# Optimization experiments

Hardware: AMD Instinct MI355X
Metric: run time of the kernel (lower is better)

Reference implementation:

```python
import jax, jax.numpy as jnp
import numpy as np

N = 50000      # nodes
E = 600000     # edges
DIN = 128      # dim_in
DOUT = 128     # dim_out (mulhead=1)
DG = 64        # dim_gate


def setup_inputs() -> dict:
    key = jax.random.key(0)
    ks = jax.random.split(key, 10)
    rows = jax.random.randint(ks[0], (E,), 0, N, dtype=jnp.int32)   # dest nodes
    cols = jax.random.randint(ks[1], (E,), 0, N, dtype=jnp.int32)   # src nodes
    vals = jax.random.uniform(ks[2], (E,), dtype=jnp.float32)       # adj_norm values
    feat = jax.random.normal(ks[3], (N, DIN), dtype=jnp.float32)
    s = 1.0 / np.sqrt(DIN)
    W0 = jax.random.normal(ks[4], (DIN, DOUT), dtype=jnp.float32) * s
    b0 = jnp.zeros((DOUT,), dtype=jnp.float32)
    W1 = jax.random.normal(ks[5], (DIN, DOUT), dtype=jnp.float32) * s
    b1 = jnp.zeros((DOUT,), dtype=jnp.float32)
    att = jax.random.normal(ks[6], (2 * DOUT,), dtype=jnp.float32) * 0.1  # attention param [1, 2*DOUT] flattened
    W_pool = jax.random.normal(ks[7], (DIN, DG), dtype=jnp.float32) * s    # weight_pool_gate
    W_gate = jax.random.normal(ks[8], (2 * DIN + DG, 1), dtype=jnp.float32) * 0.05  # weight_gate, mulhead=1
    offset0 = jnp.zeros((DOUT,), dtype=jnp.float32)
    scale0 = jnp.ones((DOUT,), dtype=jnp.float32)
    offset1 = jnp.zeros((DOUT,), dtype=jnp.float32)
    scale1 = jnp.ones((DOUT,), dtype=jnp.float32)
    return dict(rows=rows, cols=cols, vals=vals, feat=feat, W0=W0, b0=b0,
                W1=W1, b1=b1, att=att, W_pool=W_pool, W_gate=W_gate,
                offset0=offset0, scale0=scale0, offset1=offset1, scale1=scale1)


def _batch_norm(x, scale, offset):
    # per-node norm over the feature dim (unbiased=False), matching _batch_norm
    m = x.mean(axis=1, keepdims=True)
    v = x.var(axis=1, keepdims=True) + 1e-9
    return (x - m) * scale * jax.lax.rsqrt(v) + offset


def reference(rows, cols, vals, feat, W0, b0, W1, b1, att, W_pool, W_gate,
              offset0, scale0, offset1, scale1):
    n = feat.shape[0]
    d = W0.shape[1]
    # --- gate value (GaAN eq. 3) ---
    zj = feat @ W_pool                                   # [N, DG]
    neigh_zj = jax.ops.segment_max(zj[cols], rows, num_segments=n)  # per-row max over neighbors
    neigh_zj = jnp.where(jnp.isfinite(neigh_zj), neigh_zj, 0.0)     # empty rows -> zeros
    neigh_mean = jax.ops.segment_sum(vals[:, None] * feat[cols], rows, num_segments=n)  # spmm(adj, feat)
    gate = jnp.concatenate([feat, neigh_zj, neigh_mean], axis=1) @ W_gate  # [N, 1]
    # --- per-order feature transforms (order=1, mulhead=1) ---
    h0 = jax.nn.relu(feat @ W0 + b0)                     # order 0 (self)
    h1 = jax.nn.relu(feat @ W1 + b1)                     # order 1 (neighbor)
    # --- sparse attention aggregation ---
    a_self = jax.nn.leaky_relu(h0 @ att[:d], 0.2)        # [N]
    a_neigh = jax.nn.leaky_relu(h1 @ att[d:], 0.2)       # [N]
    e = a_self[rows] + a_neigh[cols]                     # per-edge score (replaces adj values)
    agg = jax.ops.segment_sum(e[:, None] * h1[cols], rows, num_segments=n)  # spmm(att_adj, h1)
    agg = agg * gate[:, :1]                              # gated
    # --- per-node batch norm, then 'mean' aggregation (sum of orders) ---
    return _batch_norm(h0, scale0, offset0) + _batch_norm(agg, scale1, offset1)
```

## Files before the change

### kernel.cpp

```cpp
#include <hip/hip_runtime.h>

#define DIN 128
#define DG 64

typedef __attribute__((ext_vector_type(8))) short short8;
typedef __attribute__((ext_vector_type(4))) float f32x4;

static __device__ __forceinline__ unsigned short f2bf(float x) {
    unsigned u = __builtin_bit_cast(unsigned, x);
    u = (u + 0x7FFF + ((u >> 16) & 1)) >> 16;
    return (unsigned short)u;
}
static __device__ __forceinline__ float bf2f(unsigned short s) {
    return __builtin_bit_cast(float, (unsigned)s << 16);
}

__global__ void k_deg(const int* __restrict__ rows, int* __restrict__ deg,
                      int* __restrict__ slot, int E) {
    int e = blockIdx.x * blockDim.x + threadIdx.x;
    if (e < E) slot[e] = atomicAdd(&deg[rows[e]], 1);
}

__global__ __launch_bounds__(1024) void k_scan1(const int* __restrict__ deg,
                                                int* __restrict__ rowptr,
                                                int* __restrict__ bsum, int n) {
    __shared__ int wsum[16];
    __shared__ int woff[16];
    int tid = threadIdx.x;
    int lane = tid & 63, w = tid >> 6;
    int i = blockIdx.x * 1024 + tid;
    int v = (i < n) ? deg[i] : 0;
    int x = v;
    #pragma unroll
    for (int off = 1; off < 64; off <<= 1) {
        int y = __shfl_up(x, off, 64);
        if (lane >= off) x += y;
    }
    if (lane == 63) wsum[w] = x;
    __syncthreads();
    if (w == 0) {
        int t = (lane < 16) ? wsum[lane] : 0;
        int xx = t;
        #pragma unroll
        for (int off = 1; off < 16; off <<= 1) {
            int y = __shfl_up(xx, off, 64);
            if (lane >= off) xx += y;
        }
        if (lane < 16) woff[lane] = xx - t;
    }
    __syncthreads();
    if (i < n) rowptr[i] = x - v + woff[w];
    if (tid == 1023) bsum[blockIdx.x] = woff[15] + wsum[15];
}

__global__ void k_scan2(const int* __restrict__ bsum, int* __restrict__ boff,
                        int* __restrict__ rowptr, int nb, int n) {
    int lane = threadIdx.x;
    int v = (lane < nb) ? bsum[lane] : 0;
    int x = v;
    #pragma unroll
    for (int off = 1; off < 64; off <<= 1) {
        int y = __shfl_up(x, off, 64);
        if (lane >= off) x += y;
    }
    boff[lane] = x - v;
    if (lane == 63) rowptr[n] = x;
}

__global__ void k_scan3(int* __restrict__ rowptr, const int* __restrict__ boff, int n) {
    int i = blockIdx.x * blockDim.x + threadIdx.x;
    if (i < n) rowptr[i] += boff[i >> 10];
}

__global__ __launch_bounds__(256) void k_prep(
    const float* __restrict__ feat, const float* __restrict__ Wg,
    unsigned short* __restrict__ featb,
    float* __restrict__ gpart, float* __restrict__ fdotg, int N, int Npad) {
    int r = blockIdx.x * 4 + (threadIdx.x >> 6);
    int lane = threadIdx.x & 63;
    if (r >= Npad) return;
    if (r >= N) {
        ((ushort2*)(featb + (size_t)r * 128))[lane] = make_ushort2(0, 0);
        return;
    }
    float2 f = ((const float2*)(feat + (size_t)r * 128))[lane];
    ((ushort2*)(featb + (size_t)r * 128))[lane] = make_ushort2(f2bf(f.x), f2bf(f.y));
    float2 G  = ((const float2*)Wg)[lane];
    float2 G2 = ((const float2*)(Wg + 192))[lane];
    float s2 = f.x * G.x + f.y * G.y;
    float s3 = f.x * G2.x + f.y * G2.y;
    #pragma unroll
    for (int off = 32; off; off >>= 1) {
        s2 += __shfl_xor(s2, off, 64);
        s3 += __shfl_xor(s3, off, 64);
    }
    if (lane == 0) { gpart[r] = s2; fdotg[r] = s3; }
}

__global__ __launch_bounds__(256) void k_wt(
    const float* __restrict__ W0, const float* __restrict__ W1,
    unsigned short* __restrict__ Bt) {
    int c = threadIdx.x;
    const float* W = (c < 128) ? W0 : W1;
    int cc = c & 127;
    for (int k = 0; k < 128; ++k)
        Bt[c * 128 + k] = f2bf(W[k * 128 + cc]);
}

#define ALD 136
__global__ __launch_bounds__(256) void k_gemm_mfma(
    const unsigned short* __restrict__ featb, const unsigned short* __restrict__ Bt,
    const float* __restrict__ b0, const float* __restrict__ b1,
    const float* __restrict__ att,
    float* __restrict__ h0, unsigned short* __restrict__ hb,
    float* __restrict__ a_self, float* __restrict__ a_neigh, int N) {
    __shared__ unsigned short As[64 * ALD];
    __shared__ float sredA[128], nredA[128];
    int tid = threadIdx.x;
    int m0 = blockIdx.x * 64;
    for (int i = tid; i < 1024; i += 256) {
        int row = i >> 4, ch = i & 15;
        uint4 v = *(const uint4*)&featb[(size_t)(m0 + row) * 128 + ch * 8];
        *(uint4*)&As[row * ALD + ch * 8] = v;
    }
    __syncthreads();
    int w = tid >> 6, lane = tid & 63;
    int lm = lane & 15, q = lane >> 4;
    f32x4 acc[4][4];
    #pragma unroll
    for (int rt = 0; rt < 4; ++rt)
        #pragma unroll
        for (int ct = 0; ct < 4; ++ct)
            #pragma unroll
            for (int r = 0; r < 4; ++r) acc[rt][ct][r] = 0.f;
    #pragma unroll
    for (int ks = 0; ks < 4; ++ks) {
        short8 a[4], b[4];
        #pragma unroll
        for (int rt = 0; rt < 4; ++rt)
            a[rt] = *(const short8*)&As[(rt * 16 + lm) * ALD + ks * 32 + q * 8];
        #pragma unroll
        for (int ct = 0; ct < 4; ++ct)
            b[ct] = *(const short8*)&Bt[(size_t)(w * 64 + ct * 16 + lm) * 128 + ks * 32 + q * 8];
        #pragma unroll
        for (int rt = 0; rt < 4; ++rt)
            #pragma unroll
            for (int ct = 0; ct < 4; ++ct)
                acc[rt][ct] = __builtin_amdgcn_mfma_f32_16x16x32_bf16(a[rt], b[ct], acc[rt][ct], 0, 0, 0);
    }
    float sacc[4][4];
    #pragma unroll
    for (int rt = 0; rt < 4; ++rt)
        #pragma unroll
        for (int r = 0; r < 4; ++r) sacc[rt][r] = 0.f;
    #pragma unroll
    for (int ct = 0; ct < 4; ++ct) {
        int col = w * 64 + ct * 16 + lm;
        float attc = att[col];
        float bias = (w < 2) ? b0[col] : b1[col - 128];
        #pragma unroll
        for (int rt = 0; rt < 4; ++rt) {
            #pragma unroll
            for (int r = 0; r < 4; ++r) {
                float v = acc[rt][ct][r] + bias;
                v = fmaxf(v, 0.f);
                sacc[rt][r] += v * attc;
                int node = m0 + rt * 16 + q * 4 + r;
                if (node < N) {
                    if (w < 2) h0[(size_t)node * 128 + col] = v;
                    else       hb[(size_t)node * 128 + (col - 128)] = f2bf(v);
                }
            }
        }
    }
    float* red = (w < 2) ? sredA : nredA;
    #pragma unroll
    for (int rt = 0; rt < 4; ++rt)
        #pragma unroll
        for (int r = 0; r < 4; ++r) {
            float s = sacc[rt][r];
            s += __shfl_xor(s, 1, 64); s += __shfl_xor(s, 2, 64);
            s += __shfl_xor(s, 4, 64); s += __shfl_xor(s, 8, 64);
            if (lm == 0) red[(w & 1) * 64 + rt * 16 + q * 4 + r] = s;
        }
    __syncthreads();
    if (tid < 64) {
        int node = m0 + tid;
        if (node < N) {
            float s  = sredA[tid] + sredA[64 + tid];
            float nn = nredA[tid] + nredA[64 + tid];
            a_self[node]  = (s  >= 0.f) ? s  : 0.2f * s;
            a_neigh[node] = (nn >= 0.f) ? nn : 0.2f * nn;
        }
    }
}

#define AS_LD 132
__global__ __launch_bounds__(256) void k_gemm_zj(
    const float* __restrict__ feat, const float* __restrict__ Wp,
    float* __restrict__ zj, int N) {
    __shared__ float As[32 * AS_LD];
    __shared__ float Bs[32 * 64];
    int tid = threadIdx.x;
    int tx = tid & 15, ty = tid >> 4;
    int m0 = blockIdx.x * 128;
    float acc[8][4];
    #pragma unroll
    for (int r = 0; r < 8; ++r)
        #pragma unroll
        for (int c = 0; c < 4; ++c) acc[r][c] = 0.f;
    for (int kc = 0; kc < 128; kc += 32) {
        for (int i = tid; i < 1024; i += 256) {
            int m = i >> 3, kq = (i & 7) << 2;
            int node = m0 + m;
            float4 f;
            if (node < N) f = *(const float4*)&feat[(size_t)node * 128 + kc + kq];
            else          f = make_float4(0.f, 0.f, 0.f, 0.f);
            As[(kq + 0) * AS_LD + m] = f.x;
            As[(kq + 1) * AS_LD + m] = f.y;
            As[(kq + 2) * AS_LD + m] = f.z;
            As[(kq + 3) * AS_LD + m] = f.w;
        }
        for (int i = tid; i < 512; i += 256) {
            int k = i >> 4, cq = (i & 15) << 2;
            *(float4*)&Bs[k * 64 + cq] = *(const float4*)&Wp[(size_t)(kc + k) * 64 + cq];
        }
        __syncthreads();
        #pragma unroll 8
        for (int kk = 0; kk < 32; ++kk) {
            const float* ar = &As[kk * AS_LD];
            float4 a0 = *(const float4*)(ar + 4 * tx);
            float4 a1 = *(const float4*)(ar + 64 + 4 * tx);
            float4 b0v = *(const float4*)&Bs[kk * 64 + 4 * ty];
            float a[8] = {a0.x, a0.y, a0.z, a0.w, a1.x, a1.y, a1.z, a1.w};
            #pragma unroll
            for (int r = 0; r < 8; ++r) {
                acc[r][0] += a[r] * b0v.x; acc[r][1] += a[r] * b0v.y;
                acc[r][2] += a[r] * b0v.z; acc[r][3] += a[r] * b0v.w;
            }
        }
        __syncthreads();
    }
    #pragma unroll
    for (int r = 0; r < 8; ++r) {
        int node = m0 + ((r < 4) ? (4 * tx + r) : (64 + 4 * tx + (r - 4)));
        if (node >= N) continue;
        *(float4*)&zj[(size_t)node * 64 + 4 * ty] =
            make_float4(acc[r][0], acc[r][1], acc[r][2], acc[r][3]);
    }
}

__global__ void k_scatter_meta(const int* __restrict__ rows, const int* __restrict__ cols,
                               const float* __restrict__ vals,
                               const int* __restrict__ rowptr, const int* __restrict__ slot,
                               const float* __restrict__ a_neigh, const float* __restrict__ fdotg,
                               float4* __restrict__ meta, int E) {
    int e = blockIdx.x * blockDim.x + threadIdx.x;
    if (e < E) {
        int c = cols[e];
        int dst = rowptr[rows[e]] + slot[e];
        meta[dst] = make_float4(__builtin_bit_cast(float, c),
                                a_neigh[c], vals[e] * fdotg[c], 0.f);
    }
}

template<int C>
static __device__ __forceinline__ void agg_chunk(
    const float4* __restrict__ meta, int j, int lane, float asr,
    const unsigned short* __restrict__ hb, const float* __restrict__ zj,
    float2& acca, float& zmax, float& vfsum) {
    float4 m[C];
    #pragma unroll
    for (int t = 0; t < C; ++t) m[t] = meta[j + t];
    ushort2 hv[C]; float zv[C];
    #pragma unroll
    for (int t = 0; t < C; ++t) {
        int c = __builtin_bit_cast(int, m[t].x);
        hv[t] = ((const ushort2*)(hb + (size_t)c * 128))[lane];
        zv[t] = zj[(size_t)c * 64 + lane];
    }
    #pragma unroll
    for (int t = 0; t < C; ++t) {
        float es = asr + m[t].y;
        acca.x += es * bf2f(hv[t].x);
        acca.y += es * bf2f(hv[t].y);
        zmax = fmaxf(zmax, zv[t]);
        vfsum += m[t].z;
    }
}

__global__ __launch_bounds__(256) void k_aggregate(
    const float4* __restrict__ meta, const int* __restrict__ rowptr,
    const float* __restrict__ h0, const unsigned short* __restrict__ hb,
    const float* __restrict__ zj,
    const float* __restrict__ a_self, const float* __restrict__ gpart,
    const float* __restrict__ Wg,
    const float* __restrict__ scale0, const float* __restrict__ offset0,
    const float* __restrict__ scale1, const float* __restrict__ offset1,
    float* __restrict__ out, int N) {
    int r = blockIdx.x * 4 + (threadIdx.x >> 6);
    int lane = threadIdx.x & 63;
    if (r >= N) return;
    int jb = rowptr[r], je = rowptr[r + 1];
    float2 acca = {0.f, 0.f};
    float zmax = -__builtin_inff();
    float vfsum = 0.f;
    float asr = a_self[r];
    int j = jb;
    while (j + 8 <= je) { agg_chunk<8>(meta, j, lane, asr, hb, zj, acca, zmax, vfsum); j += 8; }
    if (j + 4 <= je)    { agg_chunk<4>(meta, j, lane, asr, hb, zj, acca, zmax, vfsum); j += 4; }
    while (j < je)      { agg_chunk<1>(meta, j, lane, asr, hb, zj, acca, zmax, vfsum); j += 1; }
    if (jb == je) zmax = 0.f;
    float gs = zmax * Wg[128 + lane];
    #pragma unroll
    for (int off = 32; off; off >>= 1) gs += __shfl_xor(gs, off, 64);
    float gate = gpart[r] + gs + vfsum;
    float2 ag = {acca.x * gate, acca.y * gate};
    float2 x0 = ((const float2*)(h0 + (size_t)r * 128))[lane];
    float m0s = x0.x + x0.y;
    #pragma unroll
    for (int off = 32; off; off >>= 1) m0s += __shfl_xor(m0s, off, 64);
    float m0 = m0s * (1.f / 128.f);
    float d0x = x0.x - m0, d0y = x0.y - m0;
    float v0s = d0x * d0x + d0y * d0y;
    #pragma unroll
    for (int off = 32; off; off >>= 1) v0s += __shfl_xor(v0s, off, 64);
    float inv0 = rsqrtf(v0s * (1.f / 128.f) + 1e-9f);
    float m1s = ag.x + ag.y;
    #pragma unroll
    for (int off = 32; off; off >>= 1) m1s += __shfl_xor(m1s, off, 64);
    float m1 = m1s * (1.f / 128.f);
    float d1x = ag.x - m1, d1y = ag.y - m1;
    float v1s = d1x * d1x + d1y * d1y;
    #pragma unroll
    for (int off = 32; off; off >>= 1) v1s += __shfl_xor(v1s, off, 64);
    float inv1 = rsqrtf(v1s * (1.f / 128.f) + 1e-9f);
    float2 sc0 = ((const float2*)scale0)[lane], of0 = ((const float2*)offset0)[lane];
    float2 sc1 = ((const float2*)scale1)[lane], of1 = ((const float2*)offset1)[lane];
    float2 o;
    o.x = d0x * sc0.x * inv0 + of0.x + d1x * sc1.x * inv1 + of1.x;
    o.y = d0y * sc0.y * inv0 + of0.y + d1y * sc1.y * inv1 + of1.y;
    ((float2*)(out + (size_t)r * 128))[lane] = o;
}

extern "C" void kernel_launch(void* const* d_in, const int* in_sizes, int n_in,
                              void* d_out, int out_size, void* d_ws, size_t ws_size,
                              hipStream_t stream) {
    const int*   rows   = (const int*)d_in[0];
    const int*   cols   = (const int*)d_in[1];
    const float* vals   = (const float*)d_in[2];
    const float* feat   = (const float*)d_in[3];
    const float* W0     = (const float*)d_in[4];
    const float* b0     = (const float*)d_in[5];
    const float* W1     = (const float*)d_in[6];
    const float* b1     = (const float*)d_in[7];
    const float* att    = (const float*)d_in[8];
    const float* Wp     = (const float*)d_in[9];
    const float* Wg     = (const float*)d_in[10];
    const float* offset0 = (const float*)d_in[11];
    const float* scale0  = (const float*)d_in[12];
    const float* offset1 = (const float*)d_in[13];
    const float* scale1  = (const float*)d_in[14];
    float* out = (float*)d_out;

    const int E = in_sizes[0];
    const int N = in_sizes[3] / DIN;
    const int Npad = (N + 63) & ~63;

    char* ws = (char*)d_ws;
    float* h0            = (float*)ws;          ws += (size_t)N * 128 * sizeof(float);
    unsigned short* hb   = (unsigned short*)ws; ws += (size_t)N * 128 * sizeof(unsigned short);
    float* zj            = (float*)ws;          ws += (size_t)N * 64 * sizeof(float);
    unsigned short* featb = (unsigned short*)ws; ws += (size_t)Npad * 128 * sizeof(unsigned short);
    unsigned short* Bt   = (unsigned short*)ws; ws += (size_t)256 * 128 * sizeof(unsigned short);
    float* a_self  = (float*)ws; ws += (size_t)N * sizeof(float);
    float* a_neigh = (float*)ws; ws += (size_t)N * sizeof(float);
    float* gpart   = (float*)ws; ws += (size_t)N * sizeof(float);
    float* fdotg   = (float*)ws; ws += (size_t)N * sizeof(float);
    int* deg      = (int*)ws; ws += (size_t)(N + 1) * sizeof(int);
    int* rowptr   = (int*)ws; ws += (size_t)(N + 1) * sizeof(int);
    int* bsum     = (int*)ws; ws += 64 * sizeof(int);
    int* boff     = (int*)ws; ws += 64 * sizeof(int);
    int* slot     = (int*)ws; ws += (size_t)E * sizeof(int);
    ws = (char*)(((size_t)ws + 15) & ~(size_t)15);
    float4* meta  = (float4*)ws; ws += (size_t)E * sizeof(float4);

    hipMemsetAsync(deg, 0, (size_t)(N + 1) * sizeof(int), stream);

    k_deg<<<(E + 255) / 256, 256, 0, stream>>>(rows, deg, slot, E);
    int nb = (N + 1023) >> 10;
    k_scan1<<<nb, 1024, 0, stream>>>(deg, rowptr, bsum, N);
    k_scan2<<<1, 64, 0, stream>>>(bsum, boff, rowptr, nb, N);
    k_scan3<<<(N + 255) / 256, 256, 0, stream>>>(rowptr, boff, N);

    k_prep<<<Npad / 4, 256, 0, stream>>>(feat, Wg, featb, gpart, fdotg, N, Npad);
    k_wt<<<1, 256, 0, stream>>>(W0, W1, Bt);

    k_gemm_zj<<<(N + 127) / 128, 256, 0, stream>>>(feat, Wp, zj, N);
    k_gemm_mfma<<<Npad / 64, 256, 0, stream>>>(featb, Bt, b0, b1, att,
                                               h0, hb, a_self, a_neigh, N);

    k_scatter_meta<<<(E + 255) / 256, 256, 0, stream>>>(rows, cols, vals, rowptr, slot,
                                                        a_neigh, fdotg, meta, E);

    int nb4 = (N + 3) / 4;
    k_aggregate<<<nb4, 256, 0, stream>>>(meta, rowptr, h0, hb, zj,
                                         a_self, gpart, Wg,
                                         scale0, offset0, scale1, offset1, out, N);
}
```

Measured before the change: 280.8 us.

## Fuse prep, zj GEMM and MFMA GEMM into one 2D-grid kernel

Removes the k_prep kernel and the bf16 featb buffer. The MFMA GEMM now converts fp32 feat to bf16 while staging it into shared memory, and the zj GEMM also computes the gpart and fdotg gate dot products. Both GEMMs run as the two halves of one 2D-grid launch that shares one shared-memory buffer, and k_wt is spread across 128 blocks instead of one. The aggregation tail loop becomes masked chunks of 8, trading some wasted lanes on low-degree rows for less branch divergence. The goal is fewer launches and one less full pass over feat, at the cost of more fp32 global reads inside the MFMA blocks.

Result: faster. 258.4 us (-8.0%).

```diff
diff --git a/kernel.cpp b/kernel.cpp
--- a/kernel.cpp
+++ b/kernel.cpp
@@ -72,143 +72,38 @@
     if (i < n) rowptr[i] += boff[i >> 10];
 }
 
-__global__ __launch_bounds__(256) void k_prep(
-    const float* __restrict__ feat, const float* __restrict__ Wg,
-    unsigned short* __restrict__ featb,
-    float* __restrict__ gpart, float* __restrict__ fdotg, int N, int Npad) {
-    int r = blockIdx.x * 4 + (threadIdx.x >> 6);
-    int lane = threadIdx.x & 63;
-    if (r >= Npad) return;
-    if (r >= N) {
-        ((ushort2*)(featb + (size_t)r * 128))[lane] = make_ushort2(0, 0);
-        return;
-    }
-    float2 f = ((const float2*)(feat + (size_t)r * 128))[lane];
-    ((ushort2*)(featb + (size_t)r * 128))[lane] = make_ushort2(f2bf(f.x), f2bf(f.y));
-    float2 G  = ((const float2*)Wg)[lane];
-    float2 G2 = ((const float2*)(Wg + 192))[lane];
-    float s2 = f.x * G.x + f.y * G.y;
-    float s3 = f.x * G2.x + f.y * G2.y;
-    #pragma unroll
-    for (int off = 32; off; off >>= 1) {
-        s2 += __shfl_xor(s2, off, 64);
-        s3 += __shfl_xor(s3, off, 64);
-    }
-    if (lane == 0) { gpart[r] = s2; fdotg[r] = s3; }
-}
-
 __global__ __launch_bounds__(256) void k_wt(
     const float* __restrict__ W0, const float* __restrict__ W1,
     unsigned short* __restrict__ Bt) {
+    int k = blockIdx.x;
     int c = threadIdx.x;
     const float* W = (c < 128) ? W0 : W1;
-    int cc = c & 127;
-    for (int k = 0; k < 128; ++k)
-        Bt[c * 128 + k] = f2bf(W[k * 128 + cc]);
-}
-
+    Bt[c * 128 + k] = f2bf(W[k * 128 + (c & 127)]);
+}
+
+#define AS_LD 132
 #define ALD 136
-__global__ __launch_bounds__(256) void k_gemm_mfma(
-    const unsigned short* __restrict__ featb, const unsigned short* __restrict__ Bt,
-    const float* __restrict__ b0, const float* __restrict__ b1,
-    const float* __restrict__ att,
-    float* __restrict__ h0, unsigned short* __restrict__ hb,
-    float* __restrict__ a_self, float* __restrict__ a_neigh, int N) {
-    __shared__ unsigned short As[64 * ALD];
-    __shared__ float sredA[128], nredA[128];
-    int tid = threadIdx.x;
-    int m0 = blockIdx.x * 64;
-    for (int i = tid; i < 1024; i += 256) {
-        int row = i >> 4, ch = i & 15;
-        uint4 v = *(const uint4*)&featb[(size_t)(m0 + row) * 128 + ch * 8];
-        *(uint4*)&As[row * ALD + ch * 8] = v;
-    }
-    __syncthreads();
-    int w = tid >> 6, lane = tid & 63;
-    int lm = lane & 15, q = lane >> 4;
-    f32x4 acc[4][4];
-    #pragma unroll
-    for (int rt = 0; rt < 4; ++rt)
-        #pragma unroll
-        for (int ct = 0; ct < 4; ++ct)
-            #pragma unroll
-            for (int r = 0; r < 4; ++r) acc[rt][ct][r] = 0.f;
-    #pragma unroll
-    for (int ks = 0; ks < 4; ++ks) {
-        short8 a[4], b[4];
-        #pragma unroll
-        for (int rt = 0; rt < 4; ++rt)
-            a[rt] = *(const short8*)&As[(rt * 16 + lm) * ALD + ks * 32 + q * 8];
-        #pragma unroll
-        for (int ct = 0; ct < 4; ++ct)
-            b[ct] = *(const short8*)&Bt[(size_t)(w * 64 + ct * 16 + lm) * 128 + ks * 32 + q * 8];
-        #pragma unroll
-        for (int rt = 0; rt < 4; ++rt)
-            #pragma unroll
-            for (int ct = 0; ct < 4; ++ct)
-                acc[rt][ct] = __builtin_amdgcn_mfma_f32_16x16x32_bf16(a[rt], b[ct], acc[rt][ct], 0, 0, 0);
-    }
-    float sacc[4][4];
-    #pragma unroll
-    for (int rt = 0; rt < 4; ++rt)
-        #pragma unroll
-        for (int r = 0; r < 4; ++r) sacc[rt][r] = 0.f;
-    #pragma unroll
-    for (int ct = 0; ct < 4; ++ct) {
-        int col = w * 64 + ct * 16 + lm;
-        float attc = att[col];
-        float bias = (w < 2) ? b0[col] : b1[col - 128];
-        #pragma unroll
-        for (int rt = 0; rt < 4; ++rt) {
-            #pragma unroll
-            for (int r = 0; r < 4; ++r) {
-                float v = acc[rt][ct][r] + bias;
-                v = fmaxf(v, 0.f);
-                sacc[rt][r] += v * attc;
-                int node = m0 + rt * 16 + q * 4 + r;
-                if (node < N) {
-                    if (w < 2) h0[(size_t)node * 128 + col] = v;
-                    else       hb[(size_t)node * 128 + (col - 128)] = f2bf(v);
-                }
-            }
-        }
-    }
-    float* red = (w < 2) ? sredA : nredA;
-    #pragma unroll
-    for (int rt = 0; rt < 4; ++rt)
-        #pragma unroll
-        for (int r = 0; r < 4; ++r) {
-            float s = sacc[rt][r];
-            s += __shfl_xor(s, 1, 64); s += __shfl_xor(s, 2, 64);
-            s += __shfl_xor(s, 4, 64); s += __shfl_xor(s, 8, 64);
-            if (lm == 0) red[(w & 1) * 64 + rt * 16 + q * 4 + r] = s;
-        }
-    __syncthreads();
-    if (tid < 64) {
-        int node = m0 + tid;
-        if (node < N) {
-            float s  = sredA[tid] + sredA[64 + tid];
-            float nn = nredA[tid] + nredA[64 + tid];
-            a_self[node]  = (s  >= 0.f) ? s  : 0.2f * s;
-            a_neigh[node] = (nn >= 0.f) ? nn : 0.2f * nn;
-        }
-    }
-}
-
-#define AS_LD 132
-__global__ __launch_bounds__(256) void k_gemm_zj(
+#define SMEM_BYTES 25088
+
+static __device__ __forceinline__ void zj_body(
     const float* __restrict__ feat, const float* __restrict__ Wp,
-    float* __restrict__ zj, int N) {
-    __shared__ float As[32 * AS_LD];
-    __shared__ float Bs[32 * 64];
+    const float* __restrict__ Wg,
+    float* __restrict__ zj, float* __restrict__ gpart, float* __restrict__ fdotg,
+    int N, char* smem) {
+    float* As = (float*)smem;
+    float* Bs = (float*)(smem + 32 * AS_LD * 4);
     int tid = threadIdx.x;
     int tx = tid & 15, ty = tid >> 4;
     int m0 = blockIdx.x * 128;
+    if (m0 >= N) return;
     float acc[8][4];
     #pragma unroll
     for (int r = 0; r < 8; ++r)
         #pragma unroll
         for (int c = 0; c < 4; ++c) acc[r][c] = 0.f;
+    float gdot[8], fdot[8];
+    #pragma unroll
+    for (int r = 0; r < 8; ++r) { gdot[r] = 0.f; fdot[r] = 0.f; }
     for (int kc = 0; kc < 128; kc += 32) {
         for (int i = tid; i < 1024; i += 256) {
             int m = i >> 3, kq = (i & 7) << 2;
@@ -238,6 +133,10 @@
                 acc[r][0] += a[r] * b0v.x; acc[r][1] += a[r] * b0v.y;
                 acc[r][2] += a[r] * b0v.z; acc[r][3] += a[r] * b0v.w;
             }
+            float g1 = Wg[kc + kk];
+            float g2 = Wg[192 + kc + kk];
+            #pragma unroll
+            for (int r = 0; r < 8; ++r) { gdot[r] += a[r] * g1; fdot[r] += a[r] * g2; }
         }
         __syncthreads();
     }
@@ -247,7 +146,116 @@
         if (node >= N) continue;
         *(float4*)&zj[(size_t)node * 64 + 4 * ty] =
             make_float4(acc[r][0], acc[r][1], acc[r][2], acc[r][3]);
-    }
+        if (ty == 0) { gpart[node] = gdot[r]; fdotg[node] = fdot[r]; }
+    }
+}
+
+static __device__ __forceinline__ void mfma_body(
+    const float* __restrict__ feat, const unsigned short* __restrict__ Bt,
+    const float* __restrict__ b0, const float* __restrict__ b1,
+    const float* __restrict__ att,
+    float* __restrict__ h0, unsigned short* __restrict__ hb,
+    float* __restrict__ a_self, float* __restrict__ a_neigh, int N, char* smem) {
+    unsigned short* As = (unsigned short*)smem;
+    float* sredA = (float*)(smem + 64 * ALD * 2);
+    float* nredA = sredA + 128;
+    int tid = threadIdx.x;
+    int m0 = blockIdx.x * 64;
+    for (int i = tid; i < 2048; i += 256) {
+        int row = i >> 5, ch = i & 31;
+        int node = m0 + row;
+        float4 f;
+        if (node < N) f = *(const float4*)&feat[(size_t)node * 128 + ch * 4];
+        else          f = make_float4(0.f, 0.f, 0.f, 0.f);
+        unsigned p0 = (unsigned)f2bf(f.x) | ((unsigned)f2bf(f.y) << 16);
+        unsigned p1 = (unsigned)f2bf(f.z) | ((unsigned)f2bf(f.w) << 16);
+        *(uint2*)&As[row * ALD + ch * 4] = make_uint2(p0, p1);
+    }
+    __syncthreads();
+    int w = tid >> 6, lane = tid & 63;
+    int lm = lane & 15, q = lane >> 4;
+    f32x4 acc[4][4];
+    #pragma unroll
+    for (int rt = 0; rt < 4; ++rt)
+        #pragma unroll
+        for (int ct = 0; ct < 4; ++ct)
+            #pragma unroll
+            for (int r = 0; r < 4; ++r) acc[rt][ct][r] = 0.f;
+    #pragma unroll
+    for (int ks = 0; ks < 4; ++ks) {
+        short8 a[4], b[4];
+        #pragma unroll
+        for (int rt = 0; rt < 4; ++rt)
+            a[rt] = *(const short8*)&As[(rt * 16 + lm) * ALD + ks * 32 + q * 8];
+        #pragma unroll
+        for (int ct = 0; ct < 4; ++ct)
+            b[ct] = *(const short8*)&Bt[(size_t)(w * 64 + ct * 16 + lm) * 128 + ks * 32 + q * 8];
+        #pragma unroll
+        for (int rt = 0; rt < 4; ++rt)
+            #pragma unroll
+            for (int ct = 0; ct < 4; ++ct)
+                acc[rt][ct] = __builtin_amdgcn_mfma_f32_16x16x32_bf16(a[rt], b[ct], acc[rt][ct], 0, 0, 0);
+    }
+    float sacc[4][4];
+    #pragma unroll
+    for (int rt = 0; rt < 4; ++rt)
+        #pragma unroll
+        for (int r = 0; r < 4; ++r) sacc[rt][r] = 0.f;
+    #pragma unroll
+    for (int ct = 0; ct < 4; ++ct) {
+        int col = w * 64 + ct * 16 + lm;
+        float attc = att[col];
+        float bias = (w < 2) ? b0[col] : b1[col - 128];
+        #pragma unroll
+        for (int rt = 0; rt < 4; ++rt) {
+            #pragma unroll
+            for (int r = 0; r < 4; ++r) {
+                float v = acc[rt][ct][r] + bias;
+                v = fmaxf(v, 0.f);
+                sacc[rt][r] += v * attc;
+                int node = m0 + rt * 16 + q * 4 + r;
+                if (node < N) {
+                    if (w < 2) h0[(size_t)node * 128 + col] = v;
+                    else       hb[(size_t)node * 128 + (col - 128)] = f2bf(v);
+                }
+            }
+        }
+    }
+    float* red = (w < 2) ? sredA : nredA;
+    #pragma unroll
+    for (int rt = 0; rt < 4; ++rt)
+        #pragma unroll
+        for (int r = 0; r < 4; ++r) {
+            float s = sacc[rt][r];
+            s += __shfl_xor(s, 1, 64); s += __shfl_xor(s, 2, 64);
+            s += __shfl_xor(s, 4, 64); s += __shfl_xor(s, 8, 64);
+            if (lm == 0) red[(w & 1) * 64 + rt * 16 + q * 4 + r] = s;
+        }
+    __syncthreads();
+    if (tid < 64) {
+        int node = m0 + tid;
+        if (node < N) {
+            float s  = sredA[tid] + sredA[64 + tid];
+            float nn = nredA[tid] + nredA[64 + tid];
+            a_self[node]  = (s  >= 0.f) ? s  : 0.2f * s;
+            a_neigh[node] = (nn >= 0.f) ? nn : 0.2f * nn;
+        }
+    }
+}
+
+__global__ __launch_bounds__(256) void k_gemm_fused(
+    const float* __restrict__ feat, const float* __restrict__ Wp,
+    const unsigned short* __restrict__ Bt,
+    const float* __restrict__ b0, const float* __restrict__ b1,
+    const float* __restrict__ att, const float* __restrict__ Wg,
+    float* __restrict__ h0, unsigned short* __restrict__ hb,
+    float* __restrict__ zj, float* __restrict__ gpart, float* __restrict__ fdotg,
+    float* __restrict__ a_self, float* __restrict__ a_neigh, int N) {
+    __shared__ __align__(16) char smem[SMEM_BYTES];
+    if (blockIdx.y == 0)
+        zj_body(feat, Wp, Wg, zj, gpart, fdotg, N, smem);
+    else
+        mfma_body(feat, Bt, b0, b1, att, h0, hb, a_self, a_neigh, N, smem);
 }
 
 __global__ void k_scatter_meta(const int* __restrict__ rows, const int* __restrict__ cols,
@@ -265,13 +273,17 @@
 }
 
 template<int C>
-static __device__ __forceinline__ void agg_chunk(
-    const float4* __restrict__ meta, int j, int lane, float asr,
+static __device__ __forceinline__ void agg_chunk_m(
+    const float4* __restrict__ meta, int j, int je, int lane, float asr,
     const unsigned short* __restrict__ hb, const float* __restrict__ zj,
     float2& acca, float& zmax, float& vfsum) {
-    float4 m[C];
-    #pragma unroll
-    for (int t = 0; t < C; ++t) m[t] = meta[j + t];
+    float4 m[C]; bool act[C];
+    #pragma unroll
+    for (int t = 0; t < C; ++t) {
+        int jj = j + t;
+        act[t] = jj < je;
+        m[t] = meta[act[t] ? jj : (je - 1)];
+    }
     ushort2 hv[C]; float zv[C];
     #pragma unroll
     for (int t = 0; t < C; ++t) {
@@ -281,11 +293,11 @@
     }
     #pragma unroll
     for (int t = 0; t < C; ++t) {
-        float es = asr + m[t].y;
+        float es = act[t] ? (asr + m[t].y) : 0.f;
         acca.x += es * bf2f(hv[t].x);
         acca.y += es * bf2f(hv[t].y);
-        zmax = fmaxf(zmax, zv[t]);
-        vfsum += m[t].z;
+        zmax = fmaxf(zmax, act[t] ? zv[t] : -__builtin_inff());
+        vfsum += act[t] ? m[t].z : 0.f;
     }
 }
 
@@ -306,10 +318,8 @@
     float zmax = -__builtin_inff();
     float vfsum = 0.f;
     float asr = a_self[r];
-    int j = jb;
-    while (j + 8 <= je) { agg_chunk<8>(meta, j, lane, asr, hb, zj, acca, zmax, vfsum); j += 8; }
-    if (j + 4 <= je)    { agg_chunk<4>(meta, j, lane, asr, hb, zj, acca, zmax, vfsum); j += 4; }
-    while (j < je)      { agg_chunk<1>(meta, j, lane, asr, hb, zj, acca, zmax, vfsum); j += 1; }
+    for (int j = jb; j < je; j += 8)
+        agg_chunk_m<8>(meta, j, je, lane, asr, hb, zj, acca, zmax, vfsum);
     if (jb == je) zmax = 0.f;
     float gs = zmax * Wg[128 + lane];
     #pragma unroll
@@ -368,11 +378,10 @@
     const int Npad = (N + 63) & ~63;
 
     char* ws = (char*)d_ws;
-    float* h0            = (float*)ws;          ws += (size_t)N * 128 * sizeof(float);
-    unsigned short* hb   = (unsigned short*)ws; ws += (size_t)N * 128 * sizeof(unsigned short);
-    float* zj            = (float*)ws;          ws += (size_t)N * 64 * sizeof(float);
-    unsigned short* featb = (unsigned short*)ws; ws += (size_t)Npad * 128 * sizeof(unsigned short);
-    unsigned short* Bt   = (unsigned short*)ws; ws += (size_t)256 * 128 * sizeof(unsigned short);
+    float* h0          = (float*)ws;          ws += (size_t)N * 128 * sizeof(float);
+    unsigned short* hb = (unsigned short*)ws; ws += (size_t)N * 128 * sizeof(unsigned short);
+    float* zj          = (float*)ws;          ws += (size_t)N * 64 * sizeof(float);
+    unsigned short* Bt = (unsigned short*)ws; ws += (size_t)256 * 128 * sizeof(unsigned short);
     float* a_self  = (float*)ws; ws += (size_t)N * sizeof(float);
     float* a_neigh = (float*)ws; ws += (size_t)N * sizeof(float);
     float* gpart   = (float*)ws; ws += (size_t)N * sizeof(float);
@@ -393,12 +402,11 @@
     k_scan2<<<1, 64, 0, stream>>>(bsum, boff, rowptr, nb, N);
     k_scan3<<<(N + 255) / 256, 256, 0, stream>>>(rowptr, boff, N);
 
-    k_prep<<<Npad / 4, 256, 0, stream>>>(feat, Wg, featb, gpart, fdotg, N, Npad);
-    k_wt<<<1, 256, 0, stream>>>(W0, W1, Bt);
-
-    k_gemm_zj<<<(N + 127) / 128, 256, 0, stream>>>(feat, Wp, zj, N);
-    k_gemm_mfma<<<Npad / 64, 256, 0, stream>>>(featb, Bt, b0, b1, att,
-                                               h0, hb, a_self, a_neigh, N);
+    k_wt<<<128, 256, 0, stream>>>(W0, W1, Bt);
+
+    dim3 gg(Npad / 64, 2);
+    k_gemm_fused<<<gg, 256, 0, stream>>>(feat, Wp, Bt, b0, b1, att, Wg,
+                                         h0, hb, zj, gpart, fdotg, a_self, a_neigh, N);
 
     k_scatter_meta<<<(E + 255) / 256, 256, 0, stream>>>(rows, cols, vals, rowptr, slot,
                                                         a_neigh, fdotg, meta, E);
```
